# Optimization experiments

Hardware: AMD Instinct MI355X
Metric: run time of the kernel (lower is better)

The kernel has to match this reference:

```python
import jax, jax.numpy as jnp
import numpy as np

N = 50000      # nodes
E = 400000     # edges
IN = 128       # in_channels
HID = 64       # hidden_channels (per head)
H = 4          # heads
OUT = 10       # classes
G = 64         # graphs in batch


def setup_inputs() -> dict:
    key = jax.random.key(0)
    ks = jax.random.split(key, 32)
    s = 0.05
    inp = {
        "x": jax.random.normal(ks[0], (N, IN), dtype=jnp.float32),
        "edge_index": jax.random.randint(ks[1], (2, E), 0, N, dtype=jnp.int32),
        "batch": jnp.sort(jax.random.randint(ks[2], (N,), 0, G, dtype=jnp.int32)),
    }
    # TransformerConv layer 1 params (in=IN -> heads*HID)
    d1 = H * HID
    inp["Wq1"] = jax.random.normal(ks[3], (IN, d1)) * s
    inp["bq1"] = jnp.zeros((d1,), jnp.float32)
    inp["Wk1"] = jax.random.normal(ks[4], (IN, d1)) * s
    inp["bk1"] = jnp.zeros((d1,), jnp.float32)
    inp["Wv1"] = jax.random.normal(ks[5], (IN, d1)) * s
    inp["bv1"] = jnp.zeros((d1,), jnp.float32)
    inp["Ws1"] = jax.random.normal(ks[6], (IN, d1)) * s   # root/skip weight
    inp["bs1"] = jnp.zeros((d1,), jnp.float32)
    # TransformerConv layer 2 params (in=H*HID -> heads*HID)
    inp["Wq2"] = jax.random.normal(ks[7], (d1, d1)) * s
    inp["bq2"] = jnp.zeros((d1,), jnp.float32)
    inp["Wk2"] = jax.random.normal(ks[8], (d1, d1)) * s
    inp["bk2"] = jnp.zeros((d1,), jnp.float32)
    inp["Wv2"] = jax.random.normal(ks[9], (d1, d1)) * s
    inp["bv2"] = jnp.zeros((d1,), jnp.float32)
    inp["Ws2"] = jax.random.normal(ks[10], (d1, d1)) * s
    inp["bs2"] = jnp.zeros((d1,), jnp.float32)
    # final classifier
    inp["Wl"] = jax.random.normal(ks[11], (d1, OUT)) * s
    inp["bl"] = jnp.zeros((OUT,), jnp.float32)
    return inp


def transformer_conv(x, src, dst, Wq, bq, Wk, bk, Wv, bv, Ws, bs):
    """PyG TransformerConv (concat=True, root_weight=True, beta=None, eval mode).
    src = edge_index[0] (source j), dst = edge_index[1] (target i).
    """
    n = x.shape[0]
    q = (x @ Wq + bq).reshape(n, H, HID)
    k = (x @ Wk + bk).reshape(n, H, HID)
    v = (x @ Wv + bv).reshape(n, H, HID)
    # per-edge attention logits [E, H]
    alpha = jnp.einsum('ehc,ehc->eh', q[dst], k[src]) / np.sqrt(HID).astype(np.float32)
    # scatter-softmax over incoming edges of each target node
    amax = jax.ops.segment_max(alpha, dst, num_segments=n)           # [N, H], -inf for isolated
    ex = jnp.exp(alpha - amax[dst])                                   # [E, H]
    denom = jax.ops.segment_sum(ex, dst, num_segments=n) + 1e-16      # [N, H]
    w = ex / denom[dst]                                               # normalized alpha [E, H]
    # scatter-sum aggregation of weighted values
    out = jax.ops.segment_sum(w[:, :, None] * v[src], dst, num_segments=n)  # [N, H, HID]
    out = out.reshape(n, H * HID)
    return out + (x @ Ws + bs)  # root/skip connection


def reference(x, edge_index, batch,
              Wq1, bq1, Wk1, bk1, Wv1, bv1, Ws1, bs1,
              Wq2, bq2, Wk2, bk2, Wv2, bv2, Ws2, bs2,
              Wl, bl):
    src, dst = edge_index[0], edge_index[1]
    h = jax.nn.elu(transformer_conv(x, src, dst, Wq1, bq1, Wk1, bk1, Wv1, bv1, Ws1, bs1))
    h = jax.nn.elu(transformer_conv(h, src, dst, Wq2, bq2, Wk2, bk2, Wv2, bv2, Ws2, bs2))
    # global mean pool per graph
    sums = jax.ops.segment_sum(h, batch, num_segments=G)              # [G, H*HID]
    cnt = jax.ops.segment_sum(jnp.ones((h.shape[0],), h.dtype), batch, num_segments=G)
    pooled = sums / jnp.maximum(cnt, 1.0)[:, None]
    logits = pooled @ Wl + bl
    return jax.nn.log_softmax(logits, axis=-1)
```

## Files before the change

### kernel.cpp

```cpp
#include <hip/hip_runtime.h>
#include <math.h>

constexpr int NN   = 50000;
constexpr int NE   = 400000;
constexpr int INC  = 128;
constexpr int NH   = 4;
constexpr int D1   = 256;
constexpr int D4   = 1024;
constexpr int NOUT = 10;
constexpr int NG   = 64;
constexpr int NB_SCAN = (NN + 255) / 256;


typedef __attribute__((ext_vector_type(8))) short bf16x8;
typedef __attribute__((ext_vector_type(4))) float f32x4;
typedef __attribute__((ext_vector_type(2))) float f32x2;

__device__ __forceinline__ short f2b(float f) {
  union { float f; unsigned int i; } v; v.f = f;
  unsigned int x = v.i;
  return (short)((x + 0x7FFFu + ((x >> 16) & 1u)) >> 16);
}
__device__ __forceinline__ float b2f(short u) {
  union { unsigned int i; float f; } v; v.i = ((unsigned int)(unsigned short)u) << 16;
  return v.f;
}
__device__ __forceinline__ float4 ld4b(const short* p) {
  short4 u = *(const short4*)p;
  return make_float4(b2f(u.x), b2f(u.y), b2f(u.z), b2f(u.w));
}
__device__ __forceinline__ int cvt_pk_bf16(float lo, float hi) {
  int r;
  asm volatile("v_cvt_pk_bf16_f32 %0, %1, %2" : "=v"(r) : "v"(lo), "v"(hi));
  return r;
}
__device__ __forceinline__ int pk_fp8x4(float a, float b, float c, float d) {
  int v = __builtin_amdgcn_cvt_pk_fp8_f32(a, b, 0, false);
  v = __builtin_amdgcn_cvt_pk_fp8_f32(c, d, v, true);
  return v;
}

__device__ __forceinline__ void gld_lds16(const short* g, short* l) {
  __builtin_amdgcn_global_load_lds(
      (const __attribute__((address_space(1))) unsigned int*)g,
      (__attribute__((address_space(3))) unsigned int*)l, 16, 0, 0);
}

constexpr int CVT_XB  = (NN * INC / 4 + 255) / 256;
constexpr int CVT_WTB = 48;
constexpr int CVT_BB  = 8;
constexpr int CVT_DB  = (NN + 255) / 256;
constexpr int CVT_FB  = 1;
constexpr int CVT_SB  = (NG * D1 + 255) / 256;

__global__ void cvt_all_k(const float* __restrict__ x, short* __restrict__ Xb,
    const float* __restrict__ Wq1, const float* __restrict__ Wk1,
    const float* __restrict__ Wv1, const float* __restrict__ Ws1,
    const float* __restrict__ Wq2, const float* __restrict__ Wk2,
    const float* __restrict__ Wv2, const float* __restrict__ Ws2,
    short* __restrict__ Wtc1, short* __restrict__ Wtc2,
    const float* __restrict__ bq1, const float* __restrict__ bk1,
    const float* __restrict__ bv1, const float* __restrict__ bs1,
    const float* __restrict__ bq2, const float* __restrict__ bk2,
    const float* __restrict__ bv2, const float* __restrict__ bs2,
    float* __restrict__ bc1, float* __restrict__ bc2,
    int* __restrict__ deg, unsigned int* __restrict__ desc,
    float* __restrict__ sums) {
  const int b = blockIdx.x;
  const int t = threadIdx.x;
  if (b < CVT_XB) {
    int i = (b * 256 + t) * 4;
    if (i >= NN * INC) return;
    float4 v = *(const float4*)(x + i);
    short4 o; o.x = f2b(v.x); o.y = f2b(v.y); o.z = f2b(v.z); o.w = f2b(v.w);
    *(short4*)(Xb + i) = o;
  } else if (b < CVT_XB + CVT_WTB) {
    const int w = b - CVT_XB;
    const bool l1 = (w < 16);
    const int mat   = l1 ? (w >> 2) : ((w - 16) >> 3);
    const int panel = l1 ? (w & 3)  : ((w - 16) & 7);
    const int K = l1 ? INC : D1;
    const int k0 = panel * 32;
    const float* Wm[8] = {Wq1, Wk1, Wv1, Ws1, Wq2, Wk2, Wv2, Ws2};
    const float* W = Wm[(l1 ? 0 : 4) + mat];
    short* Wt = l1 ? Wtc1 : Wtc2;
    int row;
    if (mat == 0)      row = t;
    else if (mat == 3) row = 768 + t;
    else               row = 256 + (t >> 2) * 8 + ((mat == 2) ? 4 : 0) + (t & 3);
    int4 pk[4];
    short* ps = (short*)pk;
#pragma unroll
    for (int kk = 0; kk < 32; ++kk)
      ps[kk] = f2b(W[(size_t)(k0 + kk) * D1 + t]);
#pragma unroll
    for (int j = 0; j < 4; ++j)
      *(int4*)(Wt + (size_t)row * K + k0 + j * 8) = pk[j];
  } else if (b < CVT_XB + CVT_WTB + CVT_BB) {
    int i = (b - CVT_XB - CVT_WTB) * 256 + t;
    if (i >= 2 * D4) return;
    int row = i & (D4 - 1);
    const float* bq = (i < D4) ? bq1 : bq2;
    const float* bk = (i < D4) ? bk1 : bk2;
    const float* bv = (i < D4) ? bv1 : bv2;
    const float* bs = (i < D4) ? bs1 : bs2;
    float v;
    if (row < 256) v = bq[row];
    else if (row < 768) {
      int j = row - 256, grp = j >> 3, off = j & 7;
      int ch = grp * 4 + (off & 3);
      v = (off < 4) ? bk[ch] : bv[ch];
    } else v = bs[row - 768];
    ((i < D4) ? bc1 : bc2)[row] = v;
  } else if (b < CVT_XB + CVT_WTB + CVT_BB + CVT_DB) {
    int i = (b - CVT_XB - CVT_WTB - CVT_BB) * 256 + t;
    if (i < NN) deg[i] = 0;
  } else if (b < CVT_XB + CVT_WTB + CVT_BB + CVT_DB + CVT_FB) {
    if (t < NB_SCAN) desc[t] = 0u;
  } else {
    int i = (b - CVT_XB - CVT_WTB - CVT_BB - CVT_DB - CVT_FB) * 256 + t;
    if (i < NG * D1) sums[i] = 0.f;
  }
}

__global__ void deg_count(const int* __restrict__ dst, int* __restrict__ deg) {
  int e = (blockIdx.x * 256 + threadIdx.x) * 4;
  if (e + 3 < NE) {
    const int4 d = *(const int4*)(dst + e);
    atomicAdd(&deg[d.x], 1);
    atomicAdd(&deg[d.y], 1);
    atomicAdd(&deg[d.z], 1);
    atomicAdd(&deg[d.w], 1);
  } else {
    for (; e < NE; ++e) atomicAdd(&deg[dst[e]], 1);
  }
}

__global__ __launch_bounds__(256) void scan_k(const int* __restrict__ deg,
    const int* __restrict__ batch, unsigned int* __restrict__ desc,
    int* __restrict__ rowstart, int* __restrict__ cursor, int* __restrict__ gb) {
  const int b = blockIdx.x;
  const int t = threadIdx.x;
  if (b == NB_SCAN) {
    if (t > NG) return;
    int lo = 0, hi = NN;
    while (lo < hi) {
      int mid = (lo + hi) >> 1;
      if (batch[mid] < t) lo = mid + 1; else hi = mid;
    }
    gb[t] = lo;
    return;
  }
  __shared__ int sh[256];
  __shared__ int base_s;
  const int i = b * 256 + t;
  const int v = (i < NN) ? deg[i] : 0;
  sh[t] = v;
  __syncthreads();
  for (int off = 1; off < 256; off <<= 1) {
    int o = (t >= off) ? sh[t - off] : 0;
    __syncthreads();
    sh[t] += o;
    __syncthreads();
  }
  const int incl = sh[t];
  const int aggr = sh[255];
  if (t == 0)
    __hip_atomic_store(&desc[b], ((unsigned int)aggr << 2) | (b == 0 ? 2u : 1u),
                       __ATOMIC_RELEASE, __HIP_MEMORY_SCOPE_AGENT);
  if (b == 0) {
    if (t == 0) base_s = 0;
  } else if (t < 64) {
    int base = 0;
    int j = b - 1;
    for (;;) {
      const int idx = j - t;
      const unsigned int d = (idx >= 0)
          ? __hip_atomic_load(&desc[idx], __ATOMIC_ACQUIRE,
                              __HIP_MEMORY_SCOPE_AGENT)
          : 2u;
      const unsigned int st = d & 3u;
      const unsigned long long m_incl = __ballot(st == 2u);
      const unsigned long long m_inv  = __ballot(st == 0u);
      const int fi = m_incl ? (__ffsll((unsigned long long)m_incl) - 1) : 64;
      const int fv = m_inv  ? (__ffsll((unsigned long long)m_inv ) - 1) : 64;
      if (fi < fv) {
        int contrib = (t <= fi) ? (int)(d >> 2) : 0;
#pragma unroll
        for (int off = 1; off < 64; off <<= 1) contrib += __shfl_xor(contrib, off, 64);
        base += contrib;
        break;
      } else if (fv == 64) {
        int contrib = (int)(d >> 2);
#pragma unroll
        for (int off = 1; off < 64; off <<= 1) contrib += __shfl_xor(contrib, off, 64);
        base += contrib;
        j -= 64;
      } else {
        __builtin_amdgcn_s_sleep(1);
      }
    }
    if (t == 0) {
      __hip_atomic_store(&desc[b], ((unsigned int)(base + aggr) << 2) | 2u,
                         __ATOMIC_RELEASE, __HIP_MEMORY_SCOPE_AGENT);
      base_s = base;
    }
  }
  __syncthreads();
  const int excl = base_s + incl - v;
  if (i <= NN) rowstart[i] = excl;
  if (i < NN)  cursor[i]   = excl;
}

__global__ void scatter_k(const int* __restrict__ src, const int* __restrict__ dst,
    int* __restrict__ cursor, int* __restrict__ esrc) {
  int e = (blockIdx.x * 256 + threadIdx.x) * 4;
  if (e + 3 < NE) {
    const int4 s4 = *(const int4*)(src + e);
    const int4 d4 = *(const int4*)(dst + e);
    esrc[atomicAdd(&cursor[d4.x], 1)] = s4.x;
    esrc[atomicAdd(&cursor[d4.y], 1)] = s4.y;
    esrc[atomicAdd(&cursor[d4.z], 1)] = s4.z;
    esrc[atomicAdd(&cursor[d4.w], 1)] = s4.w;
  } else {
    for (; e < NE; ++e) esrc[atomicAdd(&cursor[dst[e]], 1)] = src[e];
  }
}

constexpr int CLDS = 136;

__global__ __launch_bounds__(256, 4) void gemm_mfma(
    const short* __restrict__ Xb, const short* __restrict__ Wt,
    const float* __restrict__ bias, short* __restrict__ QS,
    unsigned char* __restrict__ KV8, int M, int K) {
  __shared__ short smem[16384];
  const int bx = blockIdx.x;
  const int by = blockIdx.y;
  const int m_tile = (bx & 7) + (by << 3);
  const int n_tile = bx >> 3;
  const int m0 = m_tile * 128;
  if (m0 >= M) return;
  const int n0 = n_tile * 128;

  const int t    = threadIdx.x;
  const int lane = t & 63;
  const int wv   = t >> 6;
  const int wm   = (wv >> 1) * 64;
  const int wn   = (wv & 1) * 64;
  const int quad = lane >> 4;
  const int l16  = lane & 15;
  const int lrow = lane >> 2;
  const int lseg = lane & 3;

  const int swz_w = (lseg ^ ((lrow >> 1) & 3)) * 8;
  const int swz_r = (quad ^ ((l16 >> 1) & 3)) * 8;

  f32x4 acc[4][4] = {};

  {
#pragma unroll
    for (int j = 0; j < 2; ++j) {
      const int rb = (wv * 2 + j) * 16;
      int gm = m0 + rb + lrow;
      gm = gm < M ? gm : M - 1;
      gld_lds16(Xb + (size_t)gm * K + swz_w,              &smem[rb * 32]);
      gld_lds16(Wt + (size_t)(n0 + rb + lrow) * K + swz_w, &smem[4096 + rb * 32]);
    }
  }
  __syncthreads();

  int cur = 0;
  for (int k0 = 0; k0 < K; k0 += 32) {
    if (k0 + 32 < K) {
      short* An = &smem[(cur ^ 1) * 8192];
      short* Bn = &smem[(cur ^ 1) * 8192 + 4096];
#pragma unroll
      for (int j = 0; j < 2; ++j) {
        const int rb = (wv * 2 + j) * 16;
        int gm = m0 + rb + lrow;
        gm = gm < M ? gm : M - 1;
        gld_lds16(Xb + (size_t)gm * K + k0 + 32 + swz_w,              &An[rb * 32]);
        gld_lds16(Wt + (size_t)(n0 + rb + lrow) * K + k0 + 32 + swz_w, &Bn[rb * 32]);
      }
    }
    {
      const short* Ac = &smem[cur * 8192];
      const short* Bc = &smem[cur * 8192 + 4096];
      bf16x8 a[4], b[4];
#pragma unroll
      for (int mi = 0; mi < 4; mi++)
        a[mi] = *(const bf16x8*)(&Ac[(wm + mi * 16 + l16) * 32 + swz_r]);
#pragma unroll
      for (int nj = 0; nj < 4; nj++)
        b[nj] = *(const bf16x8*)(&Bc[(wn + nj * 16 + l16) * 32 + swz_r]);
#pragma unroll
      for (int mi = 0; mi < 4; mi++)
#pragma unroll
        for (int nj = 0; nj < 4; nj++)
          acc[mi][nj] = __builtin_amdgcn_mfma_f32_16x16x32_bf16(b[nj], a[mi], acc[mi][nj], 0, 0, 0);
    }
    __syncthreads();
    cur ^= 1;
  }

  const bool isKV = (n_tile >= 2) && (n_tile <= 5);
  float4 bz[4];
#pragma unroll
  for (int nj = 0; nj < 4; nj++)
    bz[nj] = *(const float4*)(bias + n0 + wn + nj * 16 + quad * 4);
  const int kv_base = n0 - 256;
  const int qs_base = (n_tile < 2) ? n0 : (n0 - 512);

#pragma unroll
  for (int p = 0; p < 2; ++p) {
    if ((wv >> 1) == p) {
      if (isKV) {
        unsigned char* cs = (unsigned char*)smem;
#pragma unroll
        for (int mi = 0; mi < 4; mi++) {
          const int row = mi * 16 + l16;
#pragma unroll
          for (int nj = 0; nj < 4; nj++) {
            const int colb = wn + nj * 16 + quad * 4;
            const int pk = pk_fp8x4(acc[mi][nj][0] + bz[nj].x, acc[mi][nj][1] + bz[nj].y,
                                    acc[mi][nj][2] + bz[nj].z, acc[mi][nj][3] + bz[nj].w);
            *(int*)(cs + row * 136 + colb) = pk;
          }
        }
      } else {
#pragma unroll
        for (int mi = 0; mi < 4; mi++) {
          const int row = mi * 16 + l16;
#pragma unroll
          for (int nj = 0; nj < 4; nj++) {
            const int col = wn + nj * 16 + quad * 4;
            int2 o;
            o.x = cvt_pk_bf16(acc[mi][nj][0] + bz[nj].x, acc[mi][nj][1] + bz[nj].y);
            o.y = cvt_pk_bf16(acc[mi][nj][2] + bz[nj].z, acc[mi][nj][3] + bz[nj].w);
            *(int2*)(&smem[row * CLDS + col]) = o;
          }
        }
      }
    }
    __syncthreads();
    if (isKV) {
      const unsigned char* cs = (const unsigned char*)smem;
#pragma unroll
      for (int it = 0; it < 4; ++it) {
        const int chunk = it * 256 + t;
        const int row = chunk >> 4;
        const int cb  = (chunk & 15) * 8;
        const int gm  = m0 + p * 64 + row;
        if (gm < M)
          *(int2*)(KV8 + (size_t)gm * 512 + kv_base + cb) = *(const int2*)(cs + row * 136 + cb);
      }
    } else {
#pragma unroll
      for (int it = 0; it < 4; ++it) {
        const int chunk = it * 256 + t;
        const int row = chunk >> 4;
        const int cc  = (chunk & 15) * 8;
        const int gm  = m0 + p * 64 + row;
        if (gm < M)
          *(int4*)(QS + (size_t)gm * 512 + qs_base + cc) = *(const int4*)(&smem[row * CLDS + cc]);
      }
    }
    if (p == 0) __syncthreads();
  }
}

__device__ __forceinline__ f32x2 cvt_lo(int x) { return __builtin_amdgcn_cvt_pk_f32_fp8(x, false); }
__device__ __forceinline__ f32x2 cvt_hi(int x) { return __builtin_amdgcn_cvt_pk_f32_fp8(x, true); }

template <int CTRL>
__device__ __forceinline__ float ror_add(float x) {
  int y = __builtin_amdgcn_update_dpp(0, __float_as_int(x), CTRL, 0xF, 0xF, true);
  return x + __int_as_float(y);
}
__device__ __forceinline__ float red16(float x) {
  x = ror_add<0x121>(x);
  x = ror_add<0x122>(x);
  x = ror_add<0x124>(x);
  x = ror_add<0x128>(x);
  return x;
}

#define SC2 (0.125f * 1.44269504088896341f)

__device__ __forceinline__ float edge_score(const int2 x, f32x2 q01, f32x2 q23,
                                            f32x2& vv01, f32x2& vv23) {
  f32x2 kk01 = cvt_lo(x.x), kk23 = cvt_hi(x.x);
  vv01 = cvt_lo(x.y); vv23 = cvt_hi(x.y);
  f32x2 dd = q01 * kk01;
  dd += q23 * kk23;
  return red16(dd.x + dd.y);
}

template <typename TOUT>
__device__ __forceinline__ void st1(TOUT* p, float v);
template <> __device__ __forceinline__ void st1<float>(float* p, float v) { *p = v; }
template <> __device__ __forceinline__ void st1<short>(short* p, float v) { *p = f2b(v); }

template <typename TOUT>
__global__ __launch_bounds__(256) void node_attn(
    const int* __restrict__ rowstart, const int* __restrict__ esrc,
    const short* __restrict__ QS, const unsigned char* __restrict__ KV8,
    TOUT* __restrict__ out) {
  const int nid = blockIdx.x * 4 + (threadIdx.x >> 6);
  if (nid >= NN) return;
  const int t  = threadIdx.x & 63;
  const int c0 = t * 4;
  const int r0 = __builtin_amdgcn_readfirstlane(rowstart[nid]);
  const int r1 = __builtin_amdgcn_readfirstlane(rowstart[nid + 1]);
  const short4 qu = *(const short4*)(QS + (size_t)nid * 512 + c0);
  const f32x2 q01 = {b2f(qu.x) * SC2, b2f(qu.y) * SC2};
  const f32x2 q23 = {b2f(qu.z) * SC2, b2f(qu.w) * SC2};
  const unsigned char* kvb = KV8 + t * 8;
  float denom = 0.f;
  f32x2 a01 = {0.f, 0.f}, a23 = {0.f, 0.f};
  int r = r0;
  for (; r + 7 < r1; r += 8) {
    const int e0 = __builtin_amdgcn_readfirstlane(esrc[r + 0]);
    const int e1 = __builtin_amdgcn_readfirstlane(esrc[r + 1]);
    const int e2 = __builtin_amdgcn_readfirstlane(esrc[r + 2]);
    const int e3 = __builtin_amdgcn_readfirstlane(esrc[r + 3]);
    const int e4 = __builtin_amdgcn_readfirstlane(esrc[r + 4]);
    const int e5 = __builtin_amdgcn_readfirstlane(esrc[r + 5]);
    const int e6 = __builtin_amdgcn_readfirstlane(esrc[r + 6]);
    const int e7 = __builtin_amdgcn_readfirstlane(esrc[r + 7]);
    const int2 x0 = *(const int2*)(kvb + (size_t)e0 * 512);
    const int2 x1 = *(const int2*)(kvb + (size_t)e1 * 512);
    const int2 x2 = *(const int2*)(kvb + (size_t)e2 * 512);
    const int2 x3 = *(const int2*)(kvb + (size_t)e3 * 512);
    const int2 x4 = *(const int2*)(kvb + (size_t)e4 * 512);
    const int2 x5 = *(const int2*)(kvb + (size_t)e5 * 512);
    const int2 x6 = *(const int2*)(kvb + (size_t)e6 * 512);
    const int2 x7 = *(const int2*)(kvb + (size_t)e7 * 512);
    f32x2 v01_0, v23_0, v01_1, v23_1, v01_2, v23_2, v01_3, v23_3;
    f32x2 v01_4, v23_4, v01_5, v23_5, v01_6, v23_6, v01_7, v23_7;
    const float ex0 = exp2f(edge_score(x0, q01, q23, v01_0, v23_0));
    const float ex1 = exp2f(edge_score(x1, q01, q23, v01_1, v23_1));
    const float ex2 = exp2f(edge_score(x2, q01, q23, v01_2, v23_2));
    const float ex3 = exp2f(edge_score(x3, q01, q23, v01_3, v23_3));
    const float ex4 = exp2f(edge_score(x4, q01, q23, v01_4, v23_4));
    const float ex5 = exp2f(edge_score(x5, q01, q23, v01_5, v23_5));
    const float ex6 = exp2f(edge_score(x6, q01, q23, v01_6, v23_6));
    const float ex7 = exp2f(edge_score(x7, q01, q23, v01_7, v23_7));
    denom += ((ex0 + ex1) + (ex2 + ex3)) + ((ex4 + ex5) + (ex6 + ex7));
    a01 += f32x2{ex0, ex0} * v01_0; a23 += f32x2{ex0, ex0} * v23_0;
    a01 += f32x2{ex1, ex1} * v01_1; a23 += f32x2{ex1, ex1} * v23_1;
    a01 += f32x2{ex2, ex2} * v01_2; a23 += f32x2{ex2, ex2} * v23_2;
    a01 += f32x2{ex3, ex3} * v01_3; a23 += f32x2{ex3, ex3} * v23_3;
    a01 += f32x2{ex4, ex4} * v01_4; a23 += f32x2{ex4, ex4} * v23_4;
    a01 += f32x2{ex5, ex5} * v01_5; a23 += f32x2{ex5, ex5} * v23_5;
    a01 += f32x2{ex6, ex6} * v01_6; a23 += f32x2{ex6, ex6} * v23_6;
    a01 += f32x2{ex7, ex7} * v01_7; a23 += f32x2{ex7, ex7} * v23_7;
  }
  for (; r + 3 < r1; r += 4) {
    const int e0 = __builtin_amdgcn_readfirstlane(esrc[r + 0]);
    const int e1 = __builtin_amdgcn_readfirstlane(esrc[r + 1]);
    const int e2 = __builtin_amdgcn_readfirstlane(esrc[r + 2]);
    const int e3 = __builtin_amdgcn_readfirstlane(esrc[r + 3]);
    const int2 x0 = *(const int2*)(kvb + (size_t)e0 * 512);
    const int2 x1 = *(const int2*)(kvb + (size_t)e1 * 512);
    const int2 x2 = *(const int2*)(kvb + (size_t)e2 * 512);
    const int2 x3 = *(const int2*)(kvb + (size_t)e3 * 512);
    f32x2 v01_0, v23_0, v01_1, v23_1, v01_2, v23_2, v01_3, v23_3;
    const float ex0 = exp2f(edge_score(x0, q01, q23, v01_0, v23_0));
    const float ex1 = exp2f(edge_score(x1, q01, q23, v01_1, v23_1));
    const float ex2 = exp2f(edge_score(x2, q01, q23, v01_2, v23_2));
    const float ex3 = exp2f(edge_score(x3, q01, q23, v01_3, v23_3));
    denom += (ex0 + ex1) + (ex2 + ex3);
    a01 += f32x2{ex0, ex0} * v01_0; a23 += f32x2{ex0, ex0} * v23_0;
    a01 += f32x2{ex1, ex1} * v01_1; a23 += f32x2{ex1, ex1} * v23_1;
    a01 += f32x2{ex2, ex2} * v01_2; a23 += f32x2{ex2, ex2} * v23_2;
    a01 += f32x2{ex3, ex3} * v01_3; a23 += f32x2{ex3, ex3} * v23_3;
  }
  for (; r < r1; r++) {
    const int e0 = __builtin_amdgcn_readfirstlane(esrc[r]);
    const int2 x0 = *(const int2*)(kvb + (size_t)e0 * 512);
    f32x2 v01_0, v23_0;
    const float ex0 = exp2f(edge_score(x0, q01, q23, v01_0, v23_0));
    denom += ex0;
    a01 += f32x2{ex0, ex0} * v01_0; a23 += f32x2{ex0, ex0} * v23_0;
  }
  const float inv = 1.0f / (denom + 1e-16f);
  const float4 sk = ld4b(QS + (size_t)nid * 512 + 256 + c0);
  float o0 = a01.x * inv + sk.x;
  float o1 = a01.y * inv + sk.y;
  float o2 = a23.x * inv + sk.z;
  float o3 = a23.y * inv + sk.w;
  o0 = o0 > 0.f ? o0 : expm1f(o0);
  o1 = o1 > 0.f ? o1 : expm1f(o1);
  o2 = o2 > 0.f ? o2 : expm1f(o2);
  o3 = o3 > 0.f ? o3 : expm1f(o3);
  TOUT* p = out + (size_t)nid * D1 + c0;
  st1<TOUT>(p + 0, o0); st1<TOUT>(p + 1, o1);
  st1<TOUT>(p + 2, o2); st1<TOUT>(p + 3, o3);
}

__global__ __launch_bounds__(256) void pool_k(const short* __restrict__ h,
    const int* __restrict__ batch, const int* __restrict__ gb,
    float* __restrict__ sums) {
  const int c = threadIdx.x;
  const int n0 = blockIdx.x * 64;
  const int n1 = min(n0 + 64, NN);
  const int g0 = batch[n0];
  const int g1 = batch[n1 - 1];
  for (int g = g0; g <= g1; ++g) {
    const int a = max(gb[g], n0);
    const int b = min(gb[g + 1], n1);
    if (b <= a) continue;
    float s0 = 0.f, s1 = 0.f, s2 = 0.f, s3 = 0.f;
    int n = a;
    for (; n + 3 < b; n += 4) {
      s0 += b2f(h[(size_t)(n + 0) * D1 + c]);
      s1 += b2f(h[(size_t)(n + 1) * D1 + c]);
      s2 += b2f(h[(size_t)(n + 2) * D1 + c]);
      s3 += b2f(h[(size_t)(n + 3) * D1 + c]);
    }
    for (; n < b; ++n) s0 += b2f(h[(size_t)n * D1 + c]);
    atomicAdd(&sums[(size_t)g * D1 + c], (s0 + s1) + (s2 + s3));
  }
}

__global__ __launch_bounds__(640) void head_k(const float* __restrict__ sums,
    const int* __restrict__ gb, const float* __restrict__ Wl,
    const float* __restrict__ bl, float* __restrict__ out) {
  __shared__ float logits[NG][NOUT];
  const int t = threadIdx.x;
  if (t < NG * NOUT) {
    int g = t / NOUT, o = t % NOUT;
    float inv = 1.0f / fmaxf((float)(gb[g + 1] - gb[g]), 1.0f);
    float acc = 0.f;
    for (int k = 0; k < D1; k++) acc += sums[(size_t)g * D1 + k] * Wl[k * NOUT + o];
    logits[g][o] = acc * inv + bl[o];
  }
  __syncthreads();
  if (t < NG) {
    float mx = -INFINITY;
#pragma unroll
    for (int o = 0; o < NOUT; o++) mx = fmaxf(mx, logits[t][o]);
    float s = 0.f;
#pragma unroll
    for (int o = 0; o < NOUT; o++) s += __expf(logits[t][o] - mx);
    float lse = mx + logf(s);
#pragma unroll
    for (int o = 0; o < NOUT; o++) out[t * NOUT + o] = logits[t][o] - lse;
  }
}

extern "C" void kernel_launch(void* const* d_in, const int* in_sizes, int n_in,
                              void* d_out, int out_size, void* d_ws, size_t ws_size,
                              hipStream_t stream) {
  const float* x   = (const float*)d_in[0];
  const int* ei    = (const int*)d_in[1];
  const int* batch = (const int*)d_in[2];
  const float* Wq1 = (const float*)d_in[3];  const float* bq1 = (const float*)d_in[4];
  const float* Wk1 = (const float*)d_in[5];  const float* bk1 = (const float*)d_in[6];
  const float* Wv1 = (const float*)d_in[7];  const float* bv1 = (const float*)d_in[8];
  const float* Ws1 = (const float*)d_in[9];  const float* bs1 = (const float*)d_in[10];
  const float* Wq2 = (const float*)d_in[11]; const float* bq2 = (const float*)d_in[12];
  const float* Wk2 = (const float*)d_in[13]; const float* bk2 = (const float*)d_in[14];
  const float* Wv2 = (const float*)d_in[15]; const float* bv2 = (const float*)d_in[16];
  const float* Ws2 = (const float*)d_in[17]; const float* bs2 = (const float*)d_in[18];
  const float* Wl  = (const float*)d_in[19]; const float* bl  = (const float*)d_in[20];

  const int* srcIdx = ei;
  const int* dstIdx = ei + NE;

  float* ws = (float*)d_ws;
  const size_t SZ_NODE = (size_t)NN * D1;
  short* H2b  = (short*)ws;
  float* sums = ws + SZ_NODE;
  float* bc1  = sums + (size_t)NG * D1;
  float* bc2  = bc1 + D4;
  short* Xb   = (short*)(bc2 + D4);
  short* H1b  = Xb + (size_t)NN * INC;
  short* QS   = H1b + SZ_NODE;
  short* Wtc1 = QS + (size_t)NN * 512;
  short* Wtc2 = Wtc1 + (size_t)D4 * INC;
  unsigned char* KV8 = (unsigned char*)(Wtc2 + (size_t)D4 * D1);
  int* ip      = (int*)(KV8 + (size_t)NN * 512);
  int* deg     = ip;
  unsigned int* desc = (unsigned int*)(deg + NN);
  int* rowstart= (int*)(desc + 256);
  int* cursor  = rowstart + NN + 1;
  int* esrc    = cursor + NN;
  int* gb      = esrc + NE;

  const int mtiles = (NN + 127) / 128;
  const dim3 gemmGrid(64, (mtiles + 7) / 8);
  const int edgeBlocks4 = (NE / 4 + 255) / 256;
  const int aggBlocks  = (NN + 3) / 4;
  const int cvtBlocks  = CVT_XB + CVT_WTB + CVT_BB + CVT_DB + CVT_FB + CVT_SB;

  cvt_all_k<<<cvtBlocks, 256, 0, stream>>>(x, Xb,
      Wq1, Wk1, Wv1, Ws1, Wq2, Wk2, Wv2, Ws2, Wtc1, Wtc2,
      bq1, bk1, bv1, bs1, bq2, bk2, bv2, bs2, bc1, bc2, deg, desc, sums);

  deg_count<<<edgeBlocks4, 256, 0, stream>>>(dstIdx, deg);
  scan_k<<<NB_SCAN + 1, 256, 0, stream>>>(deg, batch, desc, rowstart, cursor, gb);
  scatter_k<<<edgeBlocks4, 256, 0, stream>>>(srcIdx, dstIdx, cursor, esrc);

  gemm_mfma<<<gemmGrid, 256, 0, stream>>>(Xb, Wtc1, bc1, QS, KV8, NN, INC);
  node_attn<short><<<aggBlocks, 256, 0, stream>>>(rowstart, esrc, QS, KV8, H1b);

  gemm_mfma<<<gemmGrid, 256, 0, stream>>>(H1b, Wtc2, bc2, QS, KV8, NN, D1);
  node_attn<short><<<aggBlocks, 256, 0, stream>>>(rowstart, esrc, QS, KV8, H2b);

  pool_k<<<(NN + 63) / 64, 256, 0, stream>>>(H2b, batch, gb, sums);
  head_k<<<1, 640, 0, stream>>>(sums, gb, Wl, bl, (float*)d_out);
}
```

Measured before the change: 332.4 us.

## Triple-buffer GEMM K-loop with vmcnt waits and single-pass epilogue

Moves the MFMA GEMM from double to triple-buffered LDS staging, prefetching two K-tiles ahead. It replaces __syncthreads with explicit s_waitcnt vmcnt counts and raw s_barrier, so global-to-LDS loads overlap more compute. The epilogue now stages the whole 128x128 tile in LDS at once instead of two half passes, removing barriers. LDS grows from 32KB to 48KB, which may lower occupancy under launch_bounds(256,4), and the hand-set vmcnt values must match the number of loads in flight.

New measurement: 328.9 us. No clear change (-1.0%).

```diff
diff --git a/kernel.cpp b/kernel.cpp
--- a/kernel.cpp
+++ b/kernel.cpp
@@ -233,7 +233,7 @@
     const short* __restrict__ Xb, const short* __restrict__ Wt,
     const float* __restrict__ bias, short* __restrict__ QS,
     unsigned char* __restrict__ KV8, int M, int K) {
-  __shared__ short smem[16384];
+  __shared__ short smem[24576];
   const int bx = blockIdx.x;
   const int by = blockIdx.y;
   const int m_tile = (bx & 7) + (by << 3);
@@ -255,37 +255,39 @@
   const int swz_w = (lseg ^ ((lrow >> 1) & 3)) * 8;
   const int swz_r = (quad ^ ((l16 >> 1) & 3)) * 8;
 
-  f32x4 acc[4][4] = {};
-
-  {
+  auto stage = [&](int kt, int bi) {
+    short* A = &smem[bi * 8192];
+    short* B = &smem[bi * 8192 + 4096];
 #pragma unroll
     for (int j = 0; j < 2; ++j) {
       const int rb = (wv * 2 + j) * 16;
       int gm = m0 + rb + lrow;
       gm = gm < M ? gm : M - 1;
-      gld_lds16(Xb + (size_t)gm * K + swz_w,              &smem[rb * 32]);
-      gld_lds16(Wt + (size_t)(n0 + rb + lrow) * K + swz_w, &smem[4096 + rb * 32]);
-    }
-  }
-  __syncthreads();
-
-  int cur = 0;
+      gld_lds16(Xb + (size_t)gm * K + kt + swz_w,               &A[rb * 32]);
+      gld_lds16(Wt + (size_t)(n0 + rb + lrow) * K + kt + swz_w, &B[rb * 32]);
+    }
+  };
+
+  f32x4 acc[4][4] = {};
+
+  stage(0, 0);
+  stage(32, 1);
+
+  int bi = 0;
   for (int k0 = 0; k0 < K; k0 += 32) {
-    if (k0 + 32 < K) {
-      short* An = &smem[(cur ^ 1) * 8192];
-      short* Bn = &smem[(cur ^ 1) * 8192 + 4096];
-#pragma unroll
-      for (int j = 0; j < 2; ++j) {
-        const int rb = (wv * 2 + j) * 16;
-        int gm = m0 + rb + lrow;
-        gm = gm < M ? gm : M - 1;
-        gld_lds16(Xb + (size_t)gm * K + k0 + 32 + swz_w,              &An[rb * 32]);
-        gld_lds16(Wt + (size_t)(n0 + rb + lrow) * K + k0 + 32 + swz_w, &Bn[rb * 32]);
-      }
-    }
+    if (k0 + 64 < K) {
+      stage(k0 + 64, (bi + 2 >= 3) ? bi - 1 : bi + 2);
+      asm volatile("s_waitcnt vmcnt(8)" ::: "memory");
+    } else if (k0 + 32 < K) {
+      asm volatile("s_waitcnt vmcnt(4)" ::: "memory");
+    } else {
+      asm volatile("s_waitcnt vmcnt(0)" ::: "memory");
+    }
+    __builtin_amdgcn_s_barrier();
+    __builtin_amdgcn_sched_barrier(0);
     {
-      const short* Ac = &smem[cur * 8192];
-      const short* Bc = &smem[cur * 8192 + 4096];
+      const short* Ac = &smem[bi * 8192];
+      const short* Bc = &smem[bi * 8192 + 4096];
       bf16x8 a[4], b[4];
 #pragma unroll
       for (int mi = 0; mi < 4; mi++)
@@ -299,9 +301,11 @@
         for (int nj = 0; nj < 4; nj++)
           acc[mi][nj] = __builtin_amdgcn_mfma_f32_16x16x32_bf16(b[nj], a[mi], acc[mi][nj], 0, 0, 0);
     }
-    __syncthreads();
-    cur ^= 1;
-  }
+    __builtin_amdgcn_sched_barrier(0);
+    __builtin_amdgcn_s_barrier();
+    bi = (bi + 1 >= 3) ? 0 : bi + 1;
+  }
+  __syncthreads();
 
   const bool isKV = (n_tile >= 2) && (n_tile <= 5);
   float4 bz[4];
@@ -311,61 +315,52 @@
   const int kv_base = n0 - 256;
   const int qs_base = (n_tile < 2) ? n0 : (n0 - 512);
 
-#pragma unroll
-  for (int p = 0; p < 2; ++p) {
-    if ((wv >> 1) == p) {
-      if (isKV) {
-        unsigned char* cs = (unsigned char*)smem;
-#pragma unroll
-        for (int mi = 0; mi < 4; mi++) {
-          const int row = mi * 16 + l16;
-#pragma unroll
-          for (int nj = 0; nj < 4; nj++) {
-            const int colb = wn + nj * 16 + quad * 4;
-            const int pk = pk_fp8x4(acc[mi][nj][0] + bz[nj].x, acc[mi][nj][1] + bz[nj].y,
-                                    acc[mi][nj][2] + bz[nj].z, acc[mi][nj][3] + bz[nj].w);
-            *(int*)(cs + row * 136 + colb) = pk;
-          }
-        }
-      } else {
-#pragma unroll
-        for (int mi = 0; mi < 4; mi++) {
-          const int row = mi * 16 + l16;
-#pragma unroll
-          for (int nj = 0; nj < 4; nj++) {
-            const int col = wn + nj * 16 + quad * 4;
-            int2 o;
-            o.x = cvt_pk_bf16(acc[mi][nj][0] + bz[nj].x, acc[mi][nj][1] + bz[nj].y);
-            o.y = cvt_pk_bf16(acc[mi][nj][2] + bz[nj].z, acc[mi][nj][3] + bz[nj].w);
-            *(int2*)(&smem[row * CLDS + col]) = o;
-          }
-        }
+  if (isKV) {
+    unsigned char* cs = (unsigned char*)smem;
+#pragma unroll
+    for (int mi = 0; mi < 4; mi++) {
+      const int row = wm + mi * 16 + l16;
+#pragma unroll
+      for (int nj = 0; nj < 4; nj++) {
+        const int colb = wn + nj * 16 + quad * 4;
+        const int pk = pk_fp8x4(acc[mi][nj][0] + bz[nj].x, acc[mi][nj][1] + bz[nj].y,
+                                acc[mi][nj][2] + bz[nj].z, acc[mi][nj][3] + bz[nj].w);
+        *(int*)(cs + row * 136 + colb) = pk;
       }
     }
     __syncthreads();
-    if (isKV) {
-      const unsigned char* cs = (const unsigned char*)smem;
-#pragma unroll
-      for (int it = 0; it < 4; ++it) {
-        const int chunk = it * 256 + t;
-        const int row = chunk >> 4;
-        const int cb  = (chunk & 15) * 8;
-        const int gm  = m0 + p * 64 + row;
-        if (gm < M)
-          *(int2*)(KV8 + (size_t)gm * 512 + kv_base + cb) = *(const int2*)(cs + row * 136 + cb);
+#pragma unroll
+    for (int it = 0; it < 8; ++it) {
+      const int chunk = it * 256 + t;
+      const int row = chunk >> 4;
+      const int cb  = (chunk & 15) * 8;
+      const int gm  = m0 + row;
+      if (gm < M)
+        *(int2*)(KV8 + (size_t)gm * 512 + kv_base + cb) = *(const int2*)(cs + row * 136 + cb);
+    }
+  } else {
+#pragma unroll
+    for (int mi = 0; mi < 4; mi++) {
+      const int row = wm + mi * 16 + l16;
+#pragma unroll
+      for (int nj = 0; nj < 4; nj++) {
+        const int col = wn + nj * 16 + quad * 4;
+        int2 o;
+        o.x = cvt_pk_bf16(acc[mi][nj][0] + bz[nj].x, acc[mi][nj][1] + bz[nj].y);
+        o.y = cvt_pk_bf16(acc[mi][nj][2] + bz[nj].z, acc[mi][nj][3] + bz[nj].w);
+        *(int2*)(&smem[row * CLDS + col]) = o;
       }
-    } else {
-#pragma unroll
-      for (int it = 0; it < 4; ++it) {
-        const int chunk = it * 256 + t;
-        const int row = chunk >> 4;
-        const int cc  = (chunk & 15) * 8;
-        const int gm  = m0 + p * 64 + row;
-        if (gm < M)
-          *(int4*)(QS + (size_t)gm * 512 + qs_base + cc) = *(const int4*)(&smem[row * CLDS + cc]);
-      }
-    }
-    if (p == 0) __syncthreads();
+    }
+    __syncthreads();
+#pragma unroll
+    for (int it = 0; it < 8; ++it) {
+      const int chunk = it * 256 + t;
+      const int row = chunk >> 4;
+      const int cc  = (chunk & 15) * 8;
+      const int gm  = m0 + row;
+      if (gm < M)
+        *(int4*)(QS + (size_t)gm * 512 + qs_base + cc) = *(const int4*)(&smem[row * CLDS + cc]);
+    }
   }
 }
 
```
